# Performance work log

Hardware: AMD Instinct MI355X
Metric: run time of the kernel (lower is better)

Reference implementation:

```python
import jax, jax.numpy as jnp
import numpy as np

B, T, D = 4, 1024, 1024   # batch, seq, embed_dim
E, H = 8, 2048            # expert_count, expert_dim

def setup_inputs() -> dict:
    key = jax.random.key(0)
    ks = jax.random.split(key, 6)
    s = 0.02
    return {
        "x": jax.random.normal(ks[0], (B, T, D), dtype=jnp.float32),
        "padding_mask": jnp.zeros((B, T), dtype=bool),
        "gate_w": jax.random.normal(ks[1], (E, D), dtype=jnp.float32) * s,
        "fc1_w": jax.random.normal(ks[2], (E * H, D), dtype=jnp.float32) * s,
        "fc1_b": jax.random.normal(ks[3], (E * H,), dtype=jnp.float32) * s,
        "fc2_w": jax.random.normal(ks[4], (E * D, H), dtype=jnp.float32) * s,
        "fc2_b": jax.random.normal(ks[5], (E * D,), dtype=jnp.float32) * s,
    }

def reference(x, padding_mask, gate_w, fc1_w, fc1_b, fc2_w, fc2_b):
    b, t, d = x.shape
    e = gate_w.shape[0]
    h = fc1_w.shape[0] // e
    xf = x.reshape(b * t, d)                       # (N, D)
    pm = padding_mask.reshape(b * t)               # (N,)

    # --- Top2Gate (fp32) ---
    logits = (xf @ gate_w.T).astype(jnp.float32)   # (N, E)
    gate_value = jax.nn.softmax(logits, axis=-1)
    gate_value = jnp.where(pm[:, None], 0.0, gate_value)
    top2 = jax.lax.top_k(gate_value, 2)[1]         # (N, 2)
    sel1 = jax.nn.one_hot(top2[:, 0], e, dtype=bool)
    sel2 = jax.nn.one_hot(top2[:, 1], e, dtype=bool)
    sel = sel1 | sel2
    gw = jnp.where(sel, gate_value, 0.0)           # (N, E)
    denom = gw.sum(axis=-1, keepdims=True)
    denom = jnp.where(denom == 0, 1.0, denom)
    gate_weights = (gw / denom).astype(x.dtype)
    nt_real = (~pm).sum().astype(jnp.float32)
    top1_counts = (sel1 & ~pm[:, None]).sum(axis=0).astype(jnp.float32)  # (E,)
    lb_loss = e * ((top1_counts / nt_real) * (gate_value.sum(axis=0) / nt_real)).sum()

    # --- dense per-expert FFN ---
    a = jax.nn.relu(xf @ fc1_w.T + fc1_b)          # (N, E*H)
    a = a.reshape(-1, e, h)                        # (N, E, H)
    w2 = fc2_w.reshape(e, d, h)                    # (E, D, H)
    b2 = fc2_b.reshape(e, d)                       # (E, D)
    y = jnp.einsum('beh,edh->bed', a, w2) + b2     # (N, E, D)
    out = (y * gate_weights[:, :, None]).sum(axis=1).reshape(b, t, d)
    return out, gate_value.reshape(b, t, e), lb_loss
```

## Files before the change

kernel.cpp:

```cpp
#include <hip/hip_runtime.h>

#define NTOK 4096
#define DIM  1024
#define NEXP 8
#define HDIM 2048
#define CAP  9216

typedef unsigned short u16;
typedef __attribute__((ext_vector_type(8))) __bf16 bf16x8;
typedef __attribute__((ext_vector_type(4))) float  f32x4;
typedef __attribute__((ext_vector_type(8))) u16    u16x8;

__device__ inline u16 f2bf(float f) {
    union { float f; unsigned u; } v; v.f = f;
    unsigned r = v.u + 0x7fff + ((v.u >> 16) & 1);
    return (u16)(r >> 16);
}

__device__ inline void gload_lds16(const void* g, void* l) {
    __builtin_amdgcn_global_load_lds(
        (const __attribute__((address_space(1))) unsigned int*)g,
        (__attribute__((address_space(3))) unsigned int*)l, 16, 0, 0);
}

__global__ __launch_bounds__(256) void cvt_kernel(const float* __restrict__ in,
                                                  u16* __restrict__ out, int n8) {
    int stride = gridDim.x * 256;
    for (int i = blockIdx.x * 256 + threadIdx.x; i < n8; i += stride) {
        float4 a = ((const float4*)in)[(size_t)i * 2];
        float4 b = ((const float4*)in)[(size_t)i * 2 + 1];
        u16x8 v;
        v[0]=f2bf(a.x); v[1]=f2bf(a.y); v[2]=f2bf(a.z); v[3]=f2bf(a.w);
        v[4]=f2bf(b.x); v[5]=f2bf(b.y); v[6]=f2bf(b.z); v[7]=f2bf(b.w);
        ((u16x8*)out)[i] = v;
    }
}

__global__ __launch_bounds__(256) void gate_kernel(
    const float* __restrict__ x, const unsigned char* __restrict__ pm,
    const float* __restrict__ gw, float* __restrict__ gate_out,
    int* __restrict__ tok_e, float* __restrict__ tok_w,
    int* __restrict__ counts, float* __restrict__ gv_sum,
    float* __restrict__ top1c, float* __restrict__ nt_acc) {
    __shared__ float lgw[NEXP * DIM];
    __shared__ float bgv[NEXP];
    __shared__ float bt1[NEXP];
    __shared__ int   bcnt[NEXP];
    __shared__ float bnt;
    int t = threadIdx.x;
    for (int k = t; k < NEXP * DIM / 4; k += 256)
        ((float4*)lgw)[k] = ((const float4*)gw)[k];
    if (t < NEXP) { bgv[t] = 0.f; bt1[t] = 0.f; bcnt[t] = 0; }
    if (t == 0) bnt = 0.f;
    __syncthreads();

    int lane = t & 63, wv = t >> 6;
    for (int i = 0; i < 4; ++i) {
        int tok = blockIdx.x * 16 + wv * 4 + i;
        float acc[NEXP];
#pragma unroll
        for (int e = 0; e < NEXP; ++e) acc[e] = 0.f;
        const float* xr = x + (size_t)tok * DIM;
        for (int j = lane; j < DIM; j += 64) {
            float xv = xr[j];
#pragma unroll
            for (int e = 0; e < NEXP; ++e) acc[e] += xv * lgw[e * DIM + j];
        }
#pragma unroll
        for (int e = 0; e < NEXP; ++e) {
            float s = acc[e];
            for (int off = 1; off < 64; off <<= 1) s += __shfl_xor(s, off);
            acc[e] = s;
        }
        if (lane == 0) {
            bool padded = pm[tok] != 0;
            float m = acc[0];
            for (int e = 1; e < NEXP; ++e) m = fmaxf(m, acc[e]);
            float ex[NEXP]; float ssum = 0.f;
            for (int e = 0; e < NEXP; ++e) { ex[e] = expf(acc[e] - m); ssum += ex[e]; }
            float inv = 1.f / ssum;
            float gv[NEXP];
            for (int e = 0; e < NEXP; ++e) gv[e] = padded ? 0.f : ex[e] * inv;
            for (int e = 0; e < NEXP; ++e) gate_out[(size_t)tok * NEXP + e] = gv[e];
            int t1 = 0;
            for (int e = 1; e < NEXP; ++e) if (gv[e] > gv[t1]) t1 = e;
            int t2 = (t1 == 0) ? 1 : 0;
            for (int e = 0; e < NEXP; ++e) { if (e == t1 || e == t2) continue; if (gv[e] > gv[t2]) t2 = e; }
            float w1 = gv[t1], w2 = gv[t2], den = w1 + w2;
            float invd = (den > 0.f) ? 1.f / den : 0.f;
            tok_e[tok * 2]     = t1;  tok_e[tok * 2 + 1] = t2;
            tok_w[tok * 2]     = w1 * invd;
            tok_w[tok * 2 + 1] = w2 * invd;
            atomicAdd(&bcnt[t1], 1); atomicAdd(&bcnt[t2], 1);
            if (!padded) {
                atomicAdd(&bt1[t1], 1.f); atomicAdd(&bnt, 1.f);
                for (int e = 0; e < NEXP; ++e) atomicAdd(&bgv[e], gv[e]);
            }
        }
    }
    __syncthreads();
    if (t < NEXP) {
        atomicAdd(&counts[t], bcnt[t]);
        atomicAdd(&gv_sum[t], bgv[t]);
        atomicAdd(&top1c[t],  bt1[t]);
    }
    if (t == 0) atomicAdd(nt_acc, bnt);
}

__global__ void scan_kernel(const int* __restrict__ counts, int* __restrict__ offsets) {
    if (threadIdx.x == 0 && blockIdx.x == 0) {
        int o = 0;
        for (int e = 0; e < NEXP; ++e) { offsets[e] = o; o += (counts[e] + 127) & ~127; }
        offsets[NEXP] = o;
    }
}

__global__ __launch_bounds__(256) void scatter_kernel(
    const int* __restrict__ tok_e, const float* __restrict__ tok_w,
    const int* __restrict__ offsets, int* __restrict__ fill,
    int* __restrict__ tokens_l, float* __restrict__ gatew_l) {
    int tok = blockIdx.x * 256 + threadIdx.x;
    if (tok >= NTOK) return;
    for (int k = 0; k < 2; ++k) {
        int e = tok_e[tok * 2 + k];
        int p = atomicAdd(&fill[e], 1);
        int pos = offsets[e] + p;
        tokens_l[pos] = tok;
        gatew_l[pos]  = tok_w[tok * 2 + k];
    }
}

template <int EPI, int KDIM, int NDIM, int ASTRIDE>
__global__ __launch_bounds__(256, 2) void gemm_kernel(
    const u16* __restrict__ A, const u16* __restrict__ Bw,
    const float* __restrict__ bias,
    const int* __restrict__ tokens_l, const float* __restrict__ gatew_l,
    const int* __restrict__ counts, const int* __restrict__ offsets,
    u16* __restrict__ actout, float* __restrict__ out) {
    int e = blockIdx.z;
    int count = counts[e];
    int tm = blockIdx.y;
    if (tm * 128 >= count) return;
    int tn = blockIdx.x;
    int offs = offsets[e];

    __shared__ __align__(16) u16 lA[128 * 64];
    __shared__ __align__(16) u16 lB[128 * 64];

    int t = threadIdx.x, lane = t & 63;
    const u16* Ap[4]; const u16* Bp[4];
#pragma unroll
    for (int it = 0; it < 4; ++it) {
        int f = it * 256 + t;
        int row = f >> 3, c8 = f & 7;
        size_t arow;
        if (EPI == 1) arow = (size_t)tokens_l[offs + tm * 128 + row];
        else          arow = (size_t)(offs + tm * 128 + row);
        Ap[it] = A + arow * ASTRIDE + c8 * 8;
        Bp[it] = Bw + ((size_t)e * NDIM + tn * 128 + row) * KDIM + c8 * 8;
    }

    f32x4 acc[4][4];
#pragma unroll
    for (int i = 0; i < 4; ++i)
#pragma unroll
        for (int j = 0; j < 4; ++j) acc[i][j] = (f32x4)(0.f);

    int wm = (t >> 6) >> 1, wn = (t >> 6) & 1;
    int l16 = lane & 15, lq = lane >> 4;

    for (int kt = 0; kt < KDIM / 64; ++kt) {
#pragma unroll
        for (int it = 0; it < 4; ++it) {
            gload_lds16(Ap[it] + kt * 64, &lA[(it * 256 + t) * 8]);
            gload_lds16(Bp[it] + kt * 64, &lB[(it * 256 + t) * 8]);
        }
        asm volatile("s_waitcnt vmcnt(0)" ::: "memory");
        __syncthreads();
#pragma unroll
        for (int kk = 0; kk < 2; ++kk) {
            bf16x8 av[4], bv[4];
#pragma unroll
            for (int mi = 0; mi < 4; ++mi)
                av[mi] = *(const bf16x8*)&lA[(wm * 64 + mi * 16 + l16) * 64 + kk * 32 + lq * 8];
#pragma unroll
            for (int ni = 0; ni < 4; ++ni)
                bv[ni] = *(const bf16x8*)&lB[(wn * 64 + ni * 16 + l16) * 64 + kk * 32 + lq * 8];
#pragma unroll
            for (int mi = 0; mi < 4; ++mi)
#pragma unroll
                for (int ni = 0; ni < 4; ++ni)
                    acc[mi][ni] = __builtin_amdgcn_mfma_f32_16x16x32_bf16(av[mi], bv[ni], acc[mi][ni], 0, 0, 0);
        }
        __syncthreads();
    }

    if (EPI == 1) {
#pragma unroll
        for (int ni = 0; ni < 4; ++ni) {
            int gcol = tn * 128 + wn * 64 + ni * 16 + l16;
            float bv_ = bias[e * NDIM + gcol];
#pragma unroll
            for (int mi = 0; mi < 4; ++mi)
#pragma unroll
                for (int r = 0; r < 4; ++r) {
                    int grow = tm * 128 + wm * 64 + mi * 16 + lq * 4 + r;
                    float v = acc[mi][ni][r] + bv_;
                    v = fmaxf(v, 0.f);
                    actout[(size_t)(offs + grow) * HDIM + gcol] = f2bf(v);
                }
        }
    } else {
#pragma unroll
        for (int mi = 0; mi < 4; ++mi)
#pragma unroll
            for (int r = 0; r < 4; ++r) {
                int grow = tm * 128 + wm * 64 + mi * 16 + lq * 4 + r;
                if (grow < count) {
                    int   tk = tokens_l[offs + grow];
                    float w  = gatew_l[offs + grow];
#pragma unroll
                    for (int ni = 0; ni < 4; ++ni) {
                        int gcol = tn * 128 + wn * 64 + ni * 16 + l16;
                        float v = (acc[mi][ni][r] + bias[e * NDIM + gcol]) * w;
                        atomicAdd(&out[(size_t)tk * DIM + gcol], v);
                    }
                }
            }
    }
}

__global__ void loss_kernel(const float* __restrict__ gv_sum, const float* __restrict__ top1c,
                            const float* __restrict__ nt_acc, float* __restrict__ lout) {
    if (threadIdx.x == 0 && blockIdx.x == 0) {
        float nt = nt_acc[0];
        if (nt <= 0.f) nt = 1.f;
        float s = 0.f;
        for (int e = 0; e < NEXP; ++e) s += top1c[e] * gv_sum[e];
        lout[0] = NEXP * s / (nt * nt);
    }
}

extern "C" void kernel_launch(void* const* d_in, const int* in_sizes, int n_in,
                              void* d_out, int out_size, void* d_ws, size_t ws_size,
                              hipStream_t stream) {
    const float* x      = (const float*)d_in[0];
    const unsigned char* pm = (const unsigned char*)d_in[1];
    const float* gate_w = (const float*)d_in[2];
    const float* fc1_w  = (const float*)d_in[3];
    const float* fc1_b  = (const float*)d_in[4];
    const float* fc2_w  = (const float*)d_in[5];
    const float* fc2_b  = (const float*)d_in[6];

    float* out      = (float*)d_out;
    float* gate_out = out + (size_t)NTOK * DIM;
    float* loss_out = gate_out + (size_t)NTOK * NEXP;

    char* ws = (char*)d_ws;
    int*   counts   = (int*)ws;
    int*   fill     = counts + 8;
    float* gv_sum   = (float*)(ws + 64);
    float* top1c    = (float*)(ws + 96);
    float* nt_acc   = (float*)(ws + 128);
    int*   offsets  = (int*)(ws + 160);
    int*   tokens_l = (int*)(ws + 256);
    float* gatew_l  = (float*)(ws + 256 + CAP * 4);
    int*   tok_e    = (int*)(ws + 256 + CAP * 8);
    float* tok_w    = (float*)(ws + 256 + CAP * 8 + NTOK * 8);
    size_t off = 256 + (size_t)CAP * 8 + (size_t)NTOK * 16;
    u16* x_bf  = (u16*)(ws + off); off += (size_t)NTOK * DIM * 2;
    u16* w1_bf = (u16*)(ws + off); off += (size_t)NEXP * HDIM * DIM * 2;
    u16* w2_bf = (u16*)(ws + off); off += (size_t)NEXP * DIM * HDIM * 2;
    u16* act   = (u16*)(ws + off); off += (size_t)CAP * HDIM * 2;

    hipMemsetAsync(ws, 0, 256 + (size_t)CAP * 8, stream);
    hipMemsetAsync(d_out, 0, (size_t)NTOK * DIM * 4, stream);

    cvt_kernel<<<2048, 256, 0, stream>>>(x,     x_bf,  NTOK * DIM / 8);
    cvt_kernel<<<4096, 256, 0, stream>>>(fc1_w, w1_bf, NEXP * HDIM * DIM / 8);
    cvt_kernel<<<4096, 256, 0, stream>>>(fc2_w, w2_bf, NEXP * DIM * HDIM / 8);

    gate_kernel<<<256, 256, 0, stream>>>(x, pm, gate_w, gate_out, tok_e, tok_w,
                                         counts, gv_sum, top1c, nt_acc);
    scan_kernel<<<1, 64, 0, stream>>>(counts, offsets);
    scatter_kernel<<<16, 256, 0, stream>>>(tok_e, tok_w, offsets, fill, tokens_l, gatew_l);

    dim3 g1(16, 32, NEXP);
    gemm_kernel<1, 1024, 2048, 1024><<<g1, 256, 0, stream>>>(
        x_bf, w1_bf, fc1_b, tokens_l, gatew_l, counts, offsets, act, nullptr);
    dim3 g2(8, 32, NEXP);
    gemm_kernel<2, 2048, 1024, 2048><<<g2, 256, 0, stream>>>(
        act, w2_bf, fc2_b, tokens_l, gatew_l, counts, offsets, nullptr, out);

    loss_kernel<<<1, 64, 0, stream>>>(gv_sum, top1c, nt_acc, loss_out);
}
```

Measured before the change: 419.4 us.

## Double-buffer LDS tiles in MoE GEMMs, interleave experts in grid, fuse loss into scan

The GEMM main loop now uses two LDS buffers, so the global-to-LDS loads for the next K tile are issued before the MFMAs on the current tile run. This hides load latency and removes one barrier per iteration. The grid is flattened so expert index and N tile come from blockIdx.x, which interleaves experts across neighbouring blocks and may balance work better. The separate loss kernel is merged into the scan kernel to save one launch. LDS use doubles to 64KB per block, which may limit occupancy under launch_bounds(256,2).

After: 496.3 us. 1.18x slower.

```diff
diff --git a/kernel.cpp b/kernel.cpp
--- a/kernel.cpp
+++ b/kernel.cpp
@@ -107,11 +107,18 @@
     if (t == 0) atomicAdd(nt_acc, bnt);
 }
 
-__global__ void scan_kernel(const int* __restrict__ counts, int* __restrict__ offsets) {
+__global__ void scan_loss_kernel(const int* __restrict__ counts, int* __restrict__ offsets,
+                                 const float* __restrict__ gv_sum, const float* __restrict__ top1c,
+                                 const float* __restrict__ nt_acc, float* __restrict__ lout) {
     if (threadIdx.x == 0 && blockIdx.x == 0) {
         int o = 0;
         for (int e = 0; e < NEXP; ++e) { offsets[e] = o; o += (counts[e] + 127) & ~127; }
         offsets[NEXP] = o;
+        float nt = nt_acc[0];
+        if (nt <= 0.f) nt = 1.f;
+        float s = 0.f;
+        for (int e = 0; e < NEXP; ++e) s += top1c[e] * gv_sum[e];
+        lout[0] = NEXP * s / (nt * nt);
     }
 }
 
@@ -137,15 +144,15 @@
     const int* __restrict__ tokens_l, const float* __restrict__ gatew_l,
     const int* __restrict__ counts, const int* __restrict__ offsets,
     u16* __restrict__ actout, float* __restrict__ out) {
-    int e = blockIdx.z;
+    int e  = blockIdx.x & 7;
+    int tn = blockIdx.x >> 3;
+    int tm = blockIdx.y;
     int count = counts[e];
-    int tm = blockIdx.y;
     if (tm * 128 >= count) return;
-    int tn = blockIdx.x;
     int offs = offsets[e];
 
-    __shared__ __align__(16) u16 lA[128 * 64];
-    __shared__ __align__(16) u16 lB[128 * 64];
+    __shared__ __align__(16) u16 lA[2][128 * 64];
+    __shared__ __align__(16) u16 lB[2][128 * 64];
 
     int t = threadIdx.x, lane = t & 63;
     const u16* Ap[4]; const u16* Bp[4];
@@ -169,30 +176,55 @@
     int wm = (t >> 6) >> 1, wn = (t >> 6) & 1;
     int l16 = lane & 15, lq = lane >> 4;
 
-    for (int kt = 0; kt < KDIM / 64; ++kt) {
+    const int NKT = KDIM / 64;
+#pragma unroll
+    for (int it = 0; it < 4; ++it) {
+        gload_lds16(Ap[it], &lA[0][(it * 256 + t) * 8]);
+        gload_lds16(Bp[it], &lB[0][(it * 256 + t) * 8]);
+    }
+    asm volatile("s_waitcnt vmcnt(0)" ::: "memory");
+    __syncthreads();
+
+    int cur = 0;
+    for (int kt = 0; kt < NKT - 1; ++kt) {
 #pragma unroll
         for (int it = 0; it < 4; ++it) {
-            gload_lds16(Ap[it] + kt * 64, &lA[(it * 256 + t) * 8]);
-            gload_lds16(Bp[it] + kt * 64, &lB[(it * 256 + t) * 8]);
+            gload_lds16(Ap[it] + (kt + 1) * 64, &lA[cur ^ 1][(it * 256 + t) * 8]);
+            gload_lds16(Bp[it] + (kt + 1) * 64, &lB[cur ^ 1][(it * 256 + t) * 8]);
+        }
+#pragma unroll
+        for (int kk = 0; kk < 2; ++kk) {
+            bf16x8 av[4], bv[4];
+#pragma unroll
+            for (int mi = 0; mi < 4; ++mi)
+                av[mi] = *(const bf16x8*)&lA[cur][(wm * 64 + mi * 16 + l16) * 64 + kk * 32 + lq * 8];
+#pragma unroll
+            for (int ni = 0; ni < 4; ++ni)
+                bv[ni] = *(const bf16x8*)&lB[cur][(wn * 64 + ni * 16 + l16) * 64 + kk * 32 + lq * 8];
+#pragma unroll
+            for (int mi = 0; mi < 4; ++mi)
+#pragma unroll
+                for (int ni = 0; ni < 4; ++ni)
+                    acc[mi][ni] = __builtin_amdgcn_mfma_f32_16x16x32_bf16(av[mi], bv[ni], acc[mi][ni], 0, 0, 0);
         }
         asm volatile("s_waitcnt vmcnt(0)" ::: "memory");
         __syncthreads();
-#pragma unroll
-        for (int kk = 0; kk < 2; ++kk) {
-            bf16x8 av[4], bv[4];
-#pragma unroll
-            for (int mi = 0; mi < 4; ++mi)
-                av[mi] = *(const bf16x8*)&lA[(wm * 64 + mi * 16 + l16) * 64 + kk * 32 + lq * 8];
+        cur ^= 1;
+    }
+#pragma unroll
+    for (int kk = 0; kk < 2; ++kk) {
+        bf16x8 av[4], bv[4];
+#pragma unroll
+        for (int mi = 0; mi < 4; ++mi)
+            av[mi] = *(const bf16x8*)&lA[cur][(wm * 64 + mi * 16 + l16) * 64 + kk * 32 + lq * 8];
+#pragma unroll
+        for (int ni = 0; ni < 4; ++ni)
+            bv[ni] = *(const bf16x8*)&lB[cur][(wn * 64 + ni * 16 + l16) * 64 + kk * 32 + lq * 8];
+#pragma unroll
+        for (int mi = 0; mi < 4; ++mi)
 #pragma unroll
             for (int ni = 0; ni < 4; ++ni)
-                bv[ni] = *(const bf16x8*)&lB[(wn * 64 + ni * 16 + l16) * 64 + kk * 32 + lq * 8];
-#pragma unroll
-            for (int mi = 0; mi < 4; ++mi)
-#pragma unroll
-                for (int ni = 0; ni < 4; ++ni)
-                    acc[mi][ni] = __builtin_amdgcn_mfma_f32_16x16x32_bf16(av[mi], bv[ni], acc[mi][ni], 0, 0, 0);
-        }
-        __syncthreads();
+                acc[mi][ni] = __builtin_amdgcn_mfma_f32_16x16x32_bf16(av[mi], bv[ni], acc[mi][ni], 0, 0, 0);
     }
 
     if (EPI == 1) {
@@ -227,17 +259,6 @@
                     }
                 }
             }
-    }
-}
-
-__global__ void loss_kernel(const float* __restrict__ gv_sum, const float* __restrict__ top1c,
-                            const float* __restrict__ nt_acc, float* __restrict__ lout) {
-    if (threadIdx.x == 0 && blockIdx.x == 0) {
-        float nt = nt_acc[0];
-        if (nt <= 0.f) nt = 1.f;
-        float s = 0.f;
-        for (int e = 0; e < NEXP; ++e) s += top1c[e] * gv_sum[e];
-        lout[0] = NEXP * s / (nt * nt);
     }
 }
 
@@ -282,15 +303,13 @@
 
     gate_kernel<<<256, 256, 0, stream>>>(x, pm, gate_w, gate_out, tok_e, tok_w,
                                          counts, gv_sum, top1c, nt_acc);
-    scan_kernel<<<1, 64, 0, stream>>>(counts, offsets);
+    scan_loss_kernel<<<1, 64, 0, stream>>>(counts, offsets, gv_sum, top1c, nt_acc, loss_out);
     scatter_kernel<<<16, 256, 0, stream>>>(tok_e, tok_w, offsets, fill, tokens_l, gatew_l);
 
-    dim3 g1(16, 32, NEXP);
+    dim3 g1(8 * 16, 32);
     gemm_kernel<1, 1024, 2048, 1024><<<g1, 256, 0, stream>>>(
         x_bf, w1_bf, fc1_b, tokens_l, gatew_l, counts, offsets, act, nullptr);
-    dim3 g2(8, 32, NEXP);
+    dim3 g2(8 * 8, 32);
     gemm_kernel<2, 2048, 1024, 2048><<<g2, 256, 0, stream>>>(
         act, w2_bf, fc2_b, tokens_l, gatew_l, counts, offsets, nullptr, out);
-
-    loss_kernel<<<1, 64, 0, stream>>>(gv_sum, top1c, nt_acc, loss_out);
-}
+}
```
